# Performance work log

Measured on AMD Instinct MI355X. Metric: run time of the kernel, lower is better.

The kernel has to match this reference:

```python
import jax, jax.numpy as jnp
import numpy as np

N_NODES = 100000
N_EDGES = 1000000
IN_DIM = 128
HID1 = 64
HID2 = 64
OUT_DIM = 1
NUM_GRAPHS = 2048


def setup_inputs() -> dict:
    key = jax.random.key(0)
    ks = jax.random.split(key, 12)
    x = jax.random.normal(ks[0], (N_NODES, IN_DIM), dtype=jnp.float32)
    edge_index = jax.random.randint(ks[1], (2, N_EDGES), 0, N_NODES, dtype=jnp.int64)
    batch = jnp.sort(jax.random.randint(ks[2], (N_NODES,), 0, NUM_GRAPHS, dtype=jnp.int64))
    s1 = 1.0 / np.sqrt(IN_DIM)
    s2 = 1.0 / np.sqrt(HID1)
    s3 = 1.0 / np.sqrt(HID2)
    return {
        "x": x,
        "edge_index": edge_index,
        "batch": batch,
        "W1": jax.random.normal(ks[3], (IN_DIM, HID1), dtype=jnp.float32) * s1,
        "b1": jnp.zeros((HID1,), dtype=jnp.float32),
        "W2": jax.random.normal(ks[4], (HID1, HID2), dtype=jnp.float32) * s2,
        "b2": jnp.zeros((HID2,), dtype=jnp.float32),
        "attn_w": jax.random.normal(ks[5], (HID2, 1), dtype=jnp.float32) * s3,
        "attn_b": jnp.zeros((1,), dtype=jnp.float32),
        "mask_w": jax.random.normal(ks[6], (HID2, 1), dtype=jnp.float32) * s3,
        "mask_b": jnp.zeros((1,), dtype=jnp.float32),
        "out_w": jax.random.normal(ks[7], (HID2, OUT_DIM), dtype=jnp.float32) * s3,
        "out_b": jnp.zeros((OUT_DIM,), dtype=jnp.float32),
    }


def reference(x, edge_index, batch, W1, b1, W2, b2, attn_w, attn_b, mask_w, mask_b, out_w, out_b):
    n = x.shape[0]
    # GCNConv (PyG default): add self-loops, symmetric normalization
    loop = jnp.arange(n, dtype=edge_index.dtype)
    row = jnp.concatenate([edge_index[0], loop])  # source nodes
    col = jnp.concatenate([edge_index[1], loop])  # target nodes
    deg = jax.ops.segment_sum(jnp.ones_like(col, dtype=x.dtype), col, num_segments=n)
    dinv = jnp.where(deg > 0, jax.lax.rsqrt(jnp.maximum(deg, 1e-12)), 0.0)
    norm = dinv[row] * dinv[col]  # [E+N]

    def conv(h, W, b):
        h = h @ W                              # [N, out]
        m = h[row] * norm[:, None]             # gather + scale  [E+N, out]
        return jax.ops.segment_sum(m, col, num_segments=n) + b

    h = jax.nn.relu(conv(x, W1, b1))
    h = jax.nn.relu(conv(h, W2, b2))
    # AttentionPooling: (attn score * sigmoid mask)-weighted scatter-sum per graph
    scores = (h @ attn_w + attn_b) * jax.nn.sigmoid(h @ mask_w + mask_b)  # [N,1]
    pooled = jax.ops.segment_sum(h * scores, batch, num_segments=NUM_GRAPHS)  # [G, HID2]
    return pooled @ out_w + out_b
```

## Files before the change

### kernel.cpp

```cpp
#include <hip/hip_runtime.h>
#include <hip/hip_fp16.h>
#include <math.h>


#define NB 64
#define SEG 16
#define CAPS 80
#define SLOTS (SEG * CAPS)
#define BIN_BLOCKS 256

__device__ __forceinline__ void h8_set(float* a, const int4 w) {
    const __half2* h = (const __half2*)&w;
    float2 t0 = __half22float2(h[0]);
    float2 t1 = __half22float2(h[1]);
    float2 t2 = __half22float2(h[2]);
    float2 t3 = __half22float2(h[3]);
    a[0] = t0.x; a[1] = t0.y; a[2] = t1.x; a[3] = t1.y;
    a[4] = t2.x; a[5] = t2.y; a[6] = t3.x; a[7] = t3.y;
}
__device__ __forceinline__ void h8_acc(float* a, const int4 w) {
    const __half2* h = (const __half2*)&w;
    float2 t0 = __half22float2(h[0]);
    float2 t1 = __half22float2(h[1]);
    float2 t2 = __half22float2(h[2]);
    float2 t3 = __half22float2(h[3]);
    a[0] += t0.x; a[1] += t0.y; a[2] += t1.x; a[3] += t1.y;
    a[4] += t2.x; a[5] += t2.y; a[6] += t3.x; a[7] += t3.y;
}

__global__ __launch_bounds__(256) void gemm_bin_kernel(
    const float* __restrict__ X, const float* __restrict__ W,
    __half* __restrict__ P, int N, int K,
    const int* __restrict__ row, const int* __restrict__ col,
    int* __restrict__ bcnt, int* __restrict__ gbuf, int E,
    float* __restrict__ out, const float* __restrict__ out_b, int G) {
    __shared__ float Wl[32 * 64];
    __shared__ float xs[32 * 132];

    if (blockIdx.x < BIN_BLOCKS) {
        int seg = blockIdx.x & (SEG - 1);
        int t = blockIdx.x * 256 + threadIdx.x;
        if (t < G) out[t] = out_b[0];
        for (int e0 = t * 8; e0 < E; e0 += BIN_BLOCKS * 256 * 8) {
            if (e0 + 8 <= E) {
                int4 c0 = *(const int4*)(col + e0);
                int4 c1 = *(const int4*)(col + e0 + 4);
                int4 r0 = *(const int4*)(row + e0);
                int4 r1 = *(const int4*)(row + e0 + 4);
                int cc[8] = {c0.x, c0.y, c0.z, c0.w, c1.x, c1.y, c1.z, c1.w};
                int rr[8] = {r0.x, r0.y, r0.z, r0.w, r1.x, r1.y, r1.z, r1.w};
                int pos[8];
#pragma unroll
                for (int j = 0; j < 8; j++)
                    pos[j] = atomicAdd(&bcnt[((cc[j] >> 6) * SEG + seg) * 16], 1);
#pragma unroll
                for (int j = 0; j < 8; j++)
                    if (pos[j] < CAPS)
                        gbuf[(cc[j] >> 6) * SLOTS + seg * CAPS + pos[j]] =
                            rr[j] | ((cc[j] & 63) << 17);
            } else {
                for (int e = e0; e < E; e++) {
                    int c = col[e];
                    int b = c >> 6;
                    int pp = atomicAdd(&bcnt[(b * SEG + seg) * 16], 1);
                    if (pp < CAPS) gbuf[b * SLOTS + seg * CAPS + pp] = row[e] | ((c & 63) << 17);
                }
            }
        }
        return;
    }

    const int tid = threadIdx.x;
    const int cg = tid & 7;
    const int ng = tid >> 3;
    const int node0 = (blockIdx.x - BIN_BLOCKS) * 128;

    float acc[4][8];
#pragma unroll
    for (int r = 0; r < 4; r++)
#pragma unroll
        for (int j = 0; j < 8; j++) acc[r][j] = 0.0f;

    for (int k0 = 0; k0 < K; k0 += 32) {
        const float4* Wg = (const float4*)(W + (size_t)k0 * 64);
#pragma unroll
        for (int f = tid; f < 512; f += 256) ((float4*)Wl)[f] = Wg[f];
        {
            int rrow = tid >> 1;
            int q0 = (tid & 1) * 16;
            int node = node0 + rrow;
            const float* Xr = X + (size_t)node * K + k0 + q0;
#pragma unroll
            for (int q = 0; q < 4; q++) {
                float4 v = make_float4(0.f, 0.f, 0.f, 0.f);
                if (node < N) v = *(const float4*)(Xr + 4 * q);
                int kb = q0 + 4 * q;
                xs[(kb + 0) * 132 + rrow] = v.x;
                xs[(kb + 1) * 132 + rrow] = v.y;
                xs[(kb + 2) * 132 + rrow] = v.z;
                xs[(kb + 3) * 132 + rrow] = v.w;
            }
        }
        __syncthreads();
#pragma unroll
        for (int kk = 0; kk < 32; kk++) {
            float4 xv = *(const float4*)&xs[kk * 132 + ng * 4];
            const float* wr = &Wl[kk * 64 + cg * 8];
            float4 w0 = *(const float4*)(wr + 0);
            float4 w1 = *(const float4*)(wr + 4);
#pragma unroll
            for (int r = 0; r < 4; r++) {
                float xr = (r == 0) ? xv.x : (r == 1) ? xv.y : (r == 2) ? xv.z : xv.w;
                acc[r][0] = fmaf(xr, w0.x, acc[r][0]);
                acc[r][1] = fmaf(xr, w0.y, acc[r][1]);
                acc[r][2] = fmaf(xr, w0.z, acc[r][2]);
                acc[r][3] = fmaf(xr, w0.w, acc[r][3]);
                acc[r][4] = fmaf(xr, w1.x, acc[r][4]);
                acc[r][5] = fmaf(xr, w1.y, acc[r][5]);
                acc[r][6] = fmaf(xr, w1.z, acc[r][6]);
                acc[r][7] = fmaf(xr, w1.w, acc[r][7]);
            }
        }
        __syncthreads();
    }

#pragma unroll
    for (int r = 0; r < 4; r++) {
        int node = node0 + ng * 4 + r;
        if (node < N) {
            __half2 hh[4];
            hh[0] = __floats2half2_rn(acc[r][0], acc[r][1]);
            hh[1] = __floats2half2_rn(acc[r][2], acc[r][3]);
            hh[2] = __floats2half2_rn(acc[r][4], acc[r][5]);
            hh[3] = __floats2half2_rn(acc[r][6], acc[r][7]);
            ((int4*)(P + (size_t)node * 64))[cg] = *(int4*)hh;
        }
    }
}

__global__ __launch_bounds__(256) void sort_kernel(
    const int* __restrict__ bcnt, const int* __restrict__ gbuf,
    int* __restrict__ csr, int* __restrict__ startcnt,
    float* __restrict__ dinv, __half* __restrict__ P, int N) {
    __shared__ int scnt[SEG], segoff[SEG], s_tot;
    __shared__ int ebuf[SLOTS];
    __shared__ int lcnt[NB], lcur[NB];
    __shared__ float sdinv[NB];
    const int tid = threadIdx.x;
    const int b = blockIdx.x;
    const int base = b * SLOTS;

    if (tid < SEG) {
        int c = bcnt[(b * SEG + tid) * 16];
        scnt[tid] = c < CAPS ? c : CAPS;
    }
    if (tid < NB) lcnt[tid] = 0;
    __syncthreads();
    if (tid == 0) {
        int o = 0;
        for (int s = 0; s < SEG; s++) { segoff[s] = o; o += scnt[s]; }
        s_tot = o;
    }
    __syncthreads();
    for (int idx = tid; idx < SLOTS; idx += 256) {
        int seg = idx / CAPS;
        int j = idx - seg * CAPS;
        if (j < scnt[seg]) {
            int w = gbuf[base + idx];
            ebuf[segoff[seg] + j] = w;
            atomicAdd(&lcnt[(w >> 17) & 63], 1);
        }
    }
    __syncthreads();
    if (tid < NB) {
        int cntv = lcnt[tid];
        int rnd = (cntv + 3) & ~3;
        int val = rnd;
#pragma unroll
        for (int off = 1; off < 64; off <<= 1) {
            int n = __shfl_up(val, off, 64);
            if (tid >= off) val += n;
        }
        int st = val - rnd;
        lcur[tid] = st;
        float d = rsqrtf(1.0f + (float)cntv);
        sdinv[tid] = d;
        int v = b * NB + tid;
        if (v < N) {
            dinv[v] = d;
            int cc = cntv < 127 ? cntv : 127;
            startcnt[v] = ((base + st) << 7) | cc;
        }
    }
    __syncthreads();
    int tot = s_tot;
    for (int idx = tid; idx < tot; idx += 256) {
        int w = ebuf[idx];
        int vl = (w >> 17) & 63;
        int pp = atomicAdd(&lcur[vl], 1);
        csr[base + pp] = w & 131071;
    }
    for (int idx = tid; idx < NB * 8; idx += 256) {
        int r = idx >> 3;
        int v = b * NB + r;
        if (v < N) {
            float d = sdinv[r];
            int4* pp = (int4*)(P + (size_t)v * 64) + (idx & 7);
            int4 t = *pp;
            __half2* hp = (__half2*)&t;
#pragma unroll
            for (int q = 0; q < 4; q++) {
                float2 f = __half22float2(hp[q]);
                hp[q] = __floats2half2_rn(f.x * d, f.y * d);
            }
            *pp = t;
        }
    }
}

__global__ __launch_bounds__(256) void gather_gemm_kernel(
    const __half* __restrict__ P, const int* __restrict__ csr,
    const int* __restrict__ startcnt, const float* __restrict__ dinv,
    const float* __restrict__ b1, const float* __restrict__ W2,
    __half* __restrict__ Q, int N) {
    __shared__ float hs[64 * 65];
    __shared__ float Wl[64 * 64];
    const int tid = threadIdx.x;
    const int v0 = blockIdx.x * 64;
    const int vend = (v0 + 64 < N) ? v0 + 64 : N;
    const int p = tid & 7;

    for (int f = tid; f < 1024; f += 256)
        ((float4*)Wl)[f] = ((const float4*)W2)[f];

    const float4 bb0 = ((const float4*)b1)[2 * p];
    const float4 bb1 = ((const float4*)b1)[2 * p + 1];
    for (int v = v0 + (tid >> 3); v < vend; v += 32) {
        int pack = startcnt[v];
        int st = pack >> 7;
        int c = pack & 127;
        float dv = dinv[v];
        float a[8];
        h8_set(a, ((const int4*)(P + (size_t)v * 64))[p]);
        for (int i = 0; i < c; i += 8) {
            int4 ua = *(const int4*)(csr + st + i);
            int4 ub = *(const int4*)(csr + st + i + 4);
            int4 m0 = ((const int4*)(P + (size_t)ua.x * 64))[p];
            int4 m1 = ((const int4*)(P + (size_t)ua.y * 64))[p];
            int4 m2 = ((const int4*)(P + (size_t)ua.z * 64))[p];
            int4 m3 = ((const int4*)(P + (size_t)ua.w * 64))[p];
            int4 m4 = ((const int4*)(P + (size_t)ub.x * 64))[p];
            int4 m5 = ((const int4*)(P + (size_t)ub.y * 64))[p];
            int4 m6 = ((const int4*)(P + (size_t)ub.z * 64))[p];
            int4 m7 = ((const int4*)(P + (size_t)ub.w * 64))[p];
            h8_acc(a, m0);
            if (i + 1 < c) h8_acc(a, m1);
            if (i + 2 < c) h8_acc(a, m2);
            if (i + 3 < c) h8_acc(a, m3);
            if (i + 4 < c) h8_acc(a, m4);
            if (i + 5 < c) h8_acc(a, m5);
            if (i + 6 < c) h8_acc(a, m6);
            if (i + 7 < c) h8_acc(a, m7);
        }
        float* hd = &hs[(v - v0) * 65 + p * 8];
        hd[0] = fmaxf(fmaf(a[0], dv, bb0.x), 0.f);
        hd[1] = fmaxf(fmaf(a[1], dv, bb0.y), 0.f);
        hd[2] = fmaxf(fmaf(a[2], dv, bb0.z), 0.f);
        hd[3] = fmaxf(fmaf(a[3], dv, bb0.w), 0.f);
        hd[4] = fmaxf(fmaf(a[4], dv, bb1.x), 0.f);
        hd[5] = fmaxf(fmaf(a[5], dv, bb1.y), 0.f);
        hd[6] = fmaxf(fmaf(a[6], dv, bb1.z), 0.f);
        hd[7] = fmaxf(fmaf(a[7], dv, bb1.w), 0.f);
    }
    __syncthreads();

    const int cg = tid & 7;
    const int n0 = tid >> 3;
    float acc2[2][8];
#pragma unroll
    for (int r = 0; r < 2; r++)
#pragma unroll
        for (int j = 0; j < 8; j++) acc2[r][j] = 0.0f;
    for (int kk = 0; kk < 64; kk++) {
        float x0 = hs[(n0 * 2 + 0) * 65 + kk];
        float x1 = hs[(n0 * 2 + 1) * 65 + kk];
        const float* wr = &Wl[kk * 64 + cg * 8];
        float4 w0 = *(const float4*)(wr + 0);
        float4 w1 = *(const float4*)(wr + 4);
        acc2[0][0] = fmaf(x0, w0.x, acc2[0][0]);
        acc2[0][1] = fmaf(x0, w0.y, acc2[0][1]);
        acc2[0][2] = fmaf(x0, w0.z, acc2[0][2]);
        acc2[0][3] = fmaf(x0, w0.w, acc2[0][3]);
        acc2[0][4] = fmaf(x0, w1.x, acc2[0][4]);
        acc2[0][5] = fmaf(x0, w1.y, acc2[0][5]);
        acc2[0][6] = fmaf(x0, w1.z, acc2[0][6]);
        acc2[0][7] = fmaf(x0, w1.w, acc2[0][7]);
        acc2[1][0] = fmaf(x1, w0.x, acc2[1][0]);
        acc2[1][1] = fmaf(x1, w0.y, acc2[1][1]);
        acc2[1][2] = fmaf(x1, w0.z, acc2[1][2]);
        acc2[1][3] = fmaf(x1, w0.w, acc2[1][3]);
        acc2[1][4] = fmaf(x1, w1.x, acc2[1][4]);
        acc2[1][5] = fmaf(x1, w1.y, acc2[1][5]);
        acc2[1][6] = fmaf(x1, w1.z, acc2[1][6]);
        acc2[1][7] = fmaf(x1, w1.w, acc2[1][7]);
    }
#pragma unroll
    for (int r = 0; r < 2; r++) {
        int node = v0 + n0 * 2 + r;
        if (node < N) {
            float d = dinv[node];
            __half2 hh[4];
            hh[0] = __floats2half2_rn(acc2[r][0] * d, acc2[r][1] * d);
            hh[1] = __floats2half2_rn(acc2[r][2] * d, acc2[r][3] * d);
            hh[2] = __floats2half2_rn(acc2[r][4] * d, acc2[r][5] * d);
            hh[3] = __floats2half2_rn(acc2[r][6] * d, acc2[r][7] * d);
            ((int4*)(Q + (size_t)node * 64))[cg] = *(int4*)hh;
        }
    }
}

#define GP_NODES 64
__global__ __launch_bounds__(256) void gather_pool_kernel(
    const __half* __restrict__ Q, const int* __restrict__ csr,
    const int* __restrict__ startcnt, const float* __restrict__ dinv,
    const float* __restrict__ bias, const int* __restrict__ batch,
    const float* __restrict__ attn_w, const float* __restrict__ attn_b,
    const float* __restrict__ mask_w, const float* __restrict__ mask_b,
    const float* __restrict__ out_w, float* __restrict__ out, int N) {
    __shared__ float pacc[2048];
    __shared__ int s_gmin, s_span;
    const int tid = threadIdx.x;
    const int v0 = blockIdx.x * GP_NODES;
    const int vend = (v0 + GP_NODES < N) ? v0 + GP_NODES : N;
    if (tid == 0) {
        int gmin = batch[v0];
        s_gmin = gmin;
        s_span = batch[vend - 1] - gmin + 1;
    }
    __syncthreads();
    const int gmin = s_gmin, span = s_span;
    for (int i = tid; i < span; i += 256) pacc[i] = 0.f;
    __syncthreads();

    const int p = tid & 7;
    const float4 wa0 = ((const float4*)attn_w)[2 * p], wa1 = ((const float4*)attn_w)[2 * p + 1];
    const float4 wm0 = ((const float4*)mask_w)[2 * p], wm1 = ((const float4*)mask_w)[2 * p + 1];
    const float4 wo0 = ((const float4*)out_w)[2 * p],  wo1 = ((const float4*)out_w)[2 * p + 1];
    const float4 bb0 = ((const float4*)bias)[2 * p],   bb1 = ((const float4*)bias)[2 * p + 1];
    const float ab = attn_b[0], mb = mask_b[0];

    for (int v = v0 + (tid >> 3); v < vend; v += 32) {
        int pack = startcnt[v];
        int st = pack >> 7;
        int c = pack & 127;
        float dv = dinv[v];
        float a[8];
        h8_set(a, ((const int4*)(Q + (size_t)v * 64))[p]);
        for (int i = 0; i < c; i += 8) {
            int4 ua = *(const int4*)(csr + st + i);
            int4 ub = *(const int4*)(csr + st + i + 4);
            int4 m0 = ((const int4*)(Q + (size_t)ua.x * 64))[p];
            int4 m1 = ((const int4*)(Q + (size_t)ua.y * 64))[p];
            int4 m2 = ((const int4*)(Q + (size_t)ua.z * 64))[p];
            int4 m3 = ((const int4*)(Q + (size_t)ua.w * 64))[p];
            int4 m4 = ((const int4*)(Q + (size_t)ub.x * 64))[p];
            int4 m5 = ((const int4*)(Q + (size_t)ub.y * 64))[p];
            int4 m6 = ((const int4*)(Q + (size_t)ub.z * 64))[p];
            int4 m7 = ((const int4*)(Q + (size_t)ub.w * 64))[p];
            h8_acc(a, m0);
            if (i + 1 < c) h8_acc(a, m1);
            if (i + 2 < c) h8_acc(a, m2);
            if (i + 3 < c) h8_acc(a, m3);
            if (i + 4 < c) h8_acc(a, m4);
            if (i + 5 < c) h8_acc(a, m5);
            if (i + 6 < c) h8_acc(a, m6);
            if (i + 7 < c) h8_acc(a, m7);
        }
        float h0 = fmaxf(fmaf(a[0], dv, bb0.x), 0.f);
        float h1v = fmaxf(fmaf(a[1], dv, bb0.y), 0.f);
        float h2v = fmaxf(fmaf(a[2], dv, bb0.z), 0.f);
        float h3 = fmaxf(fmaf(a[3], dv, bb0.w), 0.f);
        float h4 = fmaxf(fmaf(a[4], dv, bb1.x), 0.f);
        float h5 = fmaxf(fmaf(a[5], dv, bb1.y), 0.f);
        float h6 = fmaxf(fmaf(a[6], dv, bb1.z), 0.f);
        float h7 = fmaxf(fmaf(a[7], dv, bb1.w), 0.f);
        float pa = h0 * wa0.x + h1v * wa0.y + h2v * wa0.z + h3 * wa0.w
                 + h4 * wa1.x + h5 * wa1.y + h6 * wa1.z + h7 * wa1.w;
        float pm = h0 * wm0.x + h1v * wm0.y + h2v * wm0.z + h3 * wm0.w
                 + h4 * wm1.x + h5 * wm1.y + h6 * wm1.z + h7 * wm1.w;
        float po = h0 * wo0.x + h1v * wo0.y + h2v * wo0.z + h3 * wo0.w
                 + h4 * wo1.x + h5 * wo1.y + h6 * wo1.z + h7 * wo1.w;
#pragma unroll
        for (int off = 1; off < 8; off <<= 1) {
            pa += __shfl_xor(pa, off, 64);
            pm += __shfl_xor(pm, off, 64);
            po += __shfl_xor(po, off, 64);
        }
        if (p == 0) {
            float cc = (pa + ab) * (1.0f / (1.0f + expf(-(pm + mb)))) * po;
            atomicAdd(&pacc[batch[v] - gmin], cc);
        }
    }
    __syncthreads();
    for (int i = tid; i < span; i += 256) {
        float val = pacc[i];
        if (val != 0.f) atomicAdd(&out[gmin + i], val);
    }
}

extern "C" void kernel_launch(void* const* d_in, const int* in_sizes, int n_in,
                              void* d_out, int out_size, void* d_ws, size_t ws_size,
                              hipStream_t stream) {
    const float* x      = (const float*)d_in[0];
    const int*   edge   = (const int*)d_in[1];
    const int*   batch  = (const int*)d_in[2];
    const float* W1     = (const float*)d_in[3];
    const float* b1     = (const float*)d_in[4];
    const float* W2     = (const float*)d_in[5];
    const float* b2     = (const float*)d_in[6];
    const float* attn_w = (const float*)d_in[7];
    const float* attn_b = (const float*)d_in[8];
    const float* mask_w = (const float*)d_in[9];
    const float* mask_b = (const float*)d_in[10];
    const float* out_w  = (const float*)d_in[11];
    const float* out_b  = (const float*)d_in[12];
    float* out = (float*)d_out;

    const int N  = in_sizes[2];
    const int E  = in_sizes[1] / 2;
    const int K1 = in_sizes[0] / N;
    const int H  = in_sizes[4];
    const int G  = out_size;
    const int* row = edge;
    const int* col = edge + E;

    const int NBUCK = (N + NB - 1) / NB;

    char* ws = (char*)d_ws;
    auto align256 = [](size_t s) { return (s + 255) / 256 * 256; };
    int*    bcnt     = (int*)ws;    ws += align256((size_t)NBUCK * SEG * 16 * 4);
    int*    gbuf     = (int*)ws;    ws += align256((size_t)NBUCK * SLOTS * 4);
    int*    csr      = (int*)ws;    ws += align256((size_t)NBUCK * SLOTS * 4);
    int*    startcnt = (int*)ws;    ws += align256((size_t)N * 4);
    float*  dinv     = (float*)ws;  ws += align256((size_t)N * 4);
    __half* P        = (__half*)ws; ws += align256((size_t)N * H * 2);
    __half* Q        = (__half*)ws;

    const int gblocks = (N + 127) / 128;

    hipMemsetAsync(bcnt, 0, (size_t)NBUCK * SEG * 16 * 4, stream);
    hipMemsetAsync(csr, 0, (size_t)NBUCK * SLOTS * 4, stream);

    gemm_bin_kernel<<<BIN_BLOCKS + gblocks, 256, 0, stream>>>(
        x, W1, P, N, K1, row, col, bcnt, gbuf, E, out, out_b, G);

    sort_kernel<<<NBUCK, 256, 0, stream>>>(bcnt, gbuf, csr, startcnt, dinv, P, N);

    gather_gemm_kernel<<<NBUCK, 256, 0, stream>>>(
        P, csr, startcnt, dinv, b1, W2, Q, N);

    gather_pool_kernel<<<NBUCK, 256, 0, stream>>>(
        Q, csr, startcnt, dinv, b2, batch, attn_w, attn_b, mask_w, mask_b, out_w, out, N);
}
```

Baseline: 238.7 us.

## Bin edges via per-block shared histogram and bulk global reservation

Replaces the per-edge global atomics on padded, segmented bucket counters with a two-pass scheme. Each of 64 binning blocks first builds a shared-memory histogram of destination buckets, reserves space with one global atomic per bucket, then scatters edges using shared atomics. The sort kernel reads a single contiguous count per bucket instead of compacting 16 segments. In exchange, each edge's column is read twice, there are fewer binning blocks, and the histogram is bounded by the Wl shared buffer size.

After: 243.3 us. About the same (+1.9%).

```diff
diff --git a/kernel.cpp b/kernel.cpp
--- a/kernel.cpp
+++ b/kernel.cpp
@@ -4,10 +4,9 @@
 
 
 #define NB 64
-#define SEG 16
-#define CAPS 80
-#define SLOTS (SEG * CAPS)
-#define BIN_BLOCKS 256
+#define SLOTS 1280
+#define BIN_BLOCKS 64
+#define MAXBUCK 2048
 
 __device__ __forceinline__ void h8_set(float* a, const int4 w) {
     const __half2* h = (const __half2*)&w;
@@ -38,34 +37,29 @@
     __shared__ float xs[32 * 132];
 
     if (blockIdx.x < BIN_BLOCKS) {
-        int seg = blockIdx.x & (SEG - 1);
-        int t = blockIdx.x * 256 + threadIdx.x;
+        int* lhist = (int*)Wl;
+        const int tid = threadIdx.x;
+        const int nbuck = (N + NB - 1) >> 6;
+        int t = blockIdx.x * 256 + tid;
         if (t < G) out[t] = out_b[0];
-        for (int e0 = t * 8; e0 < E; e0 += BIN_BLOCKS * 256 * 8) {
-            if (e0 + 8 <= E) {
-                int4 c0 = *(const int4*)(col + e0);
-                int4 c1 = *(const int4*)(col + e0 + 4);
-                int4 r0 = *(const int4*)(row + e0);
-                int4 r1 = *(const int4*)(row + e0 + 4);
-                int cc[8] = {c0.x, c0.y, c0.z, c0.w, c1.x, c1.y, c1.z, c1.w};
-                int rr[8] = {r0.x, r0.y, r0.z, r0.w, r1.x, r1.y, r1.z, r1.w};
-                int pos[8];
-#pragma unroll
-                for (int j = 0; j < 8; j++)
-                    pos[j] = atomicAdd(&bcnt[((cc[j] >> 6) * SEG + seg) * 16], 1);
-#pragma unroll
-                for (int j = 0; j < 8; j++)
-                    if (pos[j] < CAPS)
-                        gbuf[(cc[j] >> 6) * SLOTS + seg * CAPS + pos[j]] =
-                            rr[j] | ((cc[j] & 63) << 17);
-            } else {
-                for (int e = e0; e < E; e++) {
-                    int c = col[e];
-                    int b = c >> 6;
-                    int pp = atomicAdd(&bcnt[(b * SEG + seg) * 16], 1);
-                    if (pp < CAPS) gbuf[b * SLOTS + seg * CAPS + pp] = row[e] | ((c & 63) << 17);
-                }
-            }
+        for (int i = tid; i < nbuck; i += 256) lhist[i] = 0;
+        __syncthreads();
+        const int chunk = (E + BIN_BLOCKS - 1) / BIN_BLOCKS;
+        const int e0 = blockIdx.x * chunk;
+        const int e1 = (e0 + chunk < E) ? e0 + chunk : E;
+        for (int e = e0 + tid; e < e1; e += 256)
+            atomicAdd(&lhist[col[e] >> 6], 1);
+        __syncthreads();
+        for (int b = tid; b < nbuck; b += 256) {
+            int cnt = lhist[b];
+            lhist[b] = (cnt > 0) ? atomicAdd(&bcnt[b], cnt) : 0;
+        }
+        __syncthreads();
+        for (int e = e0 + tid; e < e1; e += 256) {
+            int c = col[e];
+            int b = c >> 6;
+            int p = atomicAdd(&lhist[b], 1);
+            if (p < SLOTS) gbuf[b * SLOTS + p] = row[e] | ((c & 63) << 17);
         }
         return;
     }
@@ -142,7 +136,7 @@
     const int* __restrict__ bcnt, const int* __restrict__ gbuf,
     int* __restrict__ csr, int* __restrict__ startcnt,
     float* __restrict__ dinv, __half* __restrict__ P, int N) {
-    __shared__ int scnt[SEG], segoff[SEG], s_tot;
+    __shared__ int s_tot;
     __shared__ int ebuf[SLOTS];
     __shared__ int lcnt[NB], lcur[NB];
     __shared__ float sdinv[NB];
@@ -150,26 +144,17 @@
     const int b = blockIdx.x;
     const int base = b * SLOTS;
 
-    if (tid < SEG) {
-        int c = bcnt[(b * SEG + tid) * 16];
-        scnt[tid] = c < CAPS ? c : CAPS;
+    if (tid == 0) {
+        int c = bcnt[b];
+        s_tot = c < SLOTS ? c : SLOTS;
     }
     if (tid < NB) lcnt[tid] = 0;
     __syncthreads();
-    if (tid == 0) {
-        int o = 0;
-        for (int s = 0; s < SEG; s++) { segoff[s] = o; o += scnt[s]; }
-        s_tot = o;
-    }
-    __syncthreads();
-    for (int idx = tid; idx < SLOTS; idx += 256) {
-        int seg = idx / CAPS;
-        int j = idx - seg * CAPS;
-        if (j < scnt[seg]) {
-            int w = gbuf[base + idx];
-            ebuf[segoff[seg] + j] = w;
-            atomicAdd(&lcnt[(w >> 17) & 63], 1);
-        }
+    const int tot = s_tot;
+    for (int idx = tid; idx < tot; idx += 256) {
+        int w = gbuf[base + idx];
+        ebuf[idx] = w;
+        atomicAdd(&lcnt[(w >> 17) & 63], 1);
     }
     __syncthreads();
     if (tid < NB) {
@@ -193,7 +178,6 @@
         }
     }
     __syncthreads();
-    int tot = s_tot;
     for (int idx = tid; idx < tot; idx += 256) {
         int w = ebuf[idx];
         int vl = (w >> 17) & 63;
@@ -438,7 +422,7 @@
 
     char* ws = (char*)d_ws;
     auto align256 = [](size_t s) { return (s + 255) / 256 * 256; };
-    int*    bcnt     = (int*)ws;    ws += align256((size_t)NBUCK * SEG * 16 * 4);
+    int*    bcnt     = (int*)ws;    ws += align256((size_t)NBUCK * 4);
     int*    gbuf     = (int*)ws;    ws += align256((size_t)NBUCK * SLOTS * 4);
     int*    csr      = (int*)ws;    ws += align256((size_t)NBUCK * SLOTS * 4);
     int*    startcnt = (int*)ws;    ws += align256((size_t)N * 4);
@@ -448,7 +432,7 @@
 
     const int gblocks = (N + 127) / 128;
 
-    hipMemsetAsync(bcnt, 0, (size_t)NBUCK * SEG * 16 * 4, stream);
+    hipMemsetAsync(bcnt, 0, (size_t)NBUCK * 4, stream);
     hipMemsetAsync(csr, 0, (size_t)NBUCK * SLOTS * 4, stream);
 
     gemm_bin_kernel<<<BIN_BLOCKS + gblocks, 256, 0, stream>>>(
```
